# Kernel optimization log

Hardware: AMD Instinct MI355X
Metric: run time of the kernel (lower is better)

The kernel has to match this reference:

```python
import jax, jax.numpy as jnp
import numpy as np

VOCAB = 100000
HIDDEN = 512
NUM_CLUSTERS = 256
B, S = 8, 2048


def setup_inputs() -> dict:
    key = jax.random.key(0)
    k1, k2, k3, k4, k5 = jax.random.split(key, 5)
    return {
        "location_ids": jax.random.randint(k1, (B, S), 0, VOCAB),
        "fine_embed_w": jax.random.normal(k2, (VOCAB, HIDDEN // 2), dtype=jnp.float32),
        "coarse_embed_w": jax.random.normal(k3, (NUM_CLUSTERS, HIDDEN // 2), dtype=jnp.float32),
        "loc_to_cluster_w": jax.random.normal(k4, (NUM_CLUSTERS, VOCAB), dtype=jnp.float32),
        "loc_to_cluster_b": jax.random.normal(k5, (NUM_CLUSTERS,), dtype=jnp.float32),
    }


def reference(location_ids, fine_embed_w, coarse_embed_w, loc_to_cluster_w, loc_to_cluster_b):
    # fine embedding gather: [B,S,H/2]
    fine_emb = fine_embed_w[location_ids]
    # one_hot(ids) @ W^T + b  ==  gather columns of W at ids, plus bias
    # cluster_logits: [B,S,C]
    cluster_logits = loc_to_cluster_w.T[location_ids] + loc_to_cluster_b
    cluster_dist = jax.nn.softmax(cluster_logits, axis=-1)
    # soft mixture of coarse cluster embeddings: [B,S,H/2]
    coarse_emb = jnp.einsum("bsc,ch->bsh", cluster_dist, coarse_embed_w)
    return jnp.concatenate([fine_emb, coarse_emb], axis=-1)
```

## Files before the change

### kernel.cpp

```cpp
#include <hip/hip_runtime.h>
#include <hip/hip_bf16.h>

#define VOCAB 100000
#define HALF  256
#define NC    256
#define NTOK  16384
#define SEGSZ 3200
#define NSEG  32
#define NHB   16

using frag  = __attribute__((ext_vector_type(8))) short;
using f32x4 = __attribute__((ext_vector_type(4))) float;

static __device__ inline unsigned bfpk(float lo, float hi) {
    union { __hip_bfloat162 h2; unsigned u; } cv;
    cv.h2.x = __float2bfloat16(lo);
    cv.h2.y = __float2bfloat16(hi);
    return cv.u;
}

static __device__ inline void gload_lds16(const float* g, float* l) {
    __builtin_amdgcn_global_load_lds(
        (const __attribute__((address_space(1))) void*)g,
        (__attribute__((address_space(3))) void*)l, 16, 0, 0);
}

__global__ __launch_bounds__(1024)
void prep1(const int* __restrict__ ids, const float* __restrict__ coarse_w,
           int* __restrict__ partial, ushort* __restrict__ cT)
{
    __shared__ float tile[64][65];
    __shared__ int lh[NSEG];
    const int tid = threadIdx.x;
    const int b   = blockIdx.x;

    if (b < NHB) {
        if (tid < NSEG) lh[tid] = 0;
        __syncthreads();
        atomicAdd(&lh[ids[b * 1024 + tid] / SEGSZ], 1);
        __syncthreads();
        if (tid < NSEG) partial[b * NSEG + tid] = lh[tid];
    } else {
        const int bt = b - NHB;
        const int ci = (bt >> 2) * 64, hi = (bt & 3) * 64;
#pragma unroll
        for (int p = 0; p < 4; ++p) {
            const int idx = tid + p * 1024;
            const int cl = idx >> 6, hl = idx & 63;
            tile[cl][hl] = coarse_w[(size_t)(ci + cl) * HALF + hi + hl];
        }
        __syncthreads();
#pragma unroll
        for (int p = 0; p < 4; ++p) {
            const int idx = tid + p * 1024;
            const int hl = idx >> 6, cl = idx & 63;
            __hip_bfloat16 v = __float2bfloat16(tile[cl][hl]);
            cT[(size_t)(hi + hl) * NC + ci + cl] = *reinterpret_cast<ushort*>(&v);
        }
    }
}

__global__ __launch_bounds__(1024)
void prep2(const int* __restrict__ ids, const int* __restrict__ partial,
           int* __restrict__ seg_off, int* __restrict__ stok, int* __restrict__ sidv)
{
    __shared__ int part_l[NHB][NSEG];
    __shared__ int segoff[NSEG + 1];
    __shared__ int basebs[NSEG];
    __shared__ int cnt[NSEG];
    const int tid = threadIdx.x;
    const int b   = blockIdx.x;

    if (tid < NHB * NSEG) part_l[tid >> 5][tid & 31] = partial[tid];
    __syncthreads();

    if (tid < NSEG) {
        int tot_before = 0, tot_s = 0, base = 0;
        for (int bb = 0; bb < NHB; ++bb) {
            const int v = part_l[bb][tid];
            tot_s += v;
            if (bb < b) base += v;
        }
        for (int s = 0; s < NSEG; ++s)
            if (s < tid)
                for (int bb = 0; bb < NHB; ++bb) tot_before += part_l[bb][s];
        segoff[tid] = tot_before;
        basebs[tid] = base;
        cnt[tid]    = 0;
        if (tid == NSEG - 1) segoff[NSEG] = tot_before + tot_s;
    }
    __syncthreads();

    const int t  = b * 1024 + tid;
    const int id = ids[t];
    const int sg = id / SEGSZ;
    const int r  = atomicAdd(&cnt[sg], 1);
    const int pos = segoff[sg] + basebs[sg] + r;
    stok[pos] = t;
    sidv[pos] = id;

    if (b == 0 && tid <= NSEG) seg_off[tid] = segoff[tid];
}

__global__ __launch_bounds__(256)
void gather_rows(const float* __restrict__ cluster_w,
                 const float* __restrict__ cluster_b,
                 const int*   __restrict__ sidv,
                 const int*   __restrict__ seg_off,
                 __hip_bfloat16* __restrict__ logT)
{
    __shared__ float seg[3328];
    const int bid  = blockIdx.x;
    const int r    = bid >> 5;
    const int s    = bid & 31;
    const int tid  = threadIdx.x;
    const int wave = tid >> 6;
    const int lane = tid & 63;
    const int sbase = s * SEGSZ;

    const float* rowseg = cluster_w + (size_t)r * VOCAB + sbase;

    if (r == NC - 1 && s == NSEG - 1) {
        const int nf4 = (VOCAB - sbase) >> 2;
        for (int i = tid; i < nf4; i += 256)
            *reinterpret_cast<float4*>(&seg[4 * i]) =
                reinterpret_cast<const float4*>(rowseg)[i];
    } else {
        gload_lds16(rowseg + (wave)      * 256 + lane * 4, &seg[(wave)      * 256]);
        gload_lds16(rowseg + (wave + 4)  * 256 + lane * 4, &seg[(wave + 4)  * 256]);
        gload_lds16(rowseg + (wave + 8)  * 256 + lane * 4, &seg[(wave + 8)  * 256]);
        if (wave == 0)
            gload_lds16(rowseg + 12 * 256 + lane * 4, &seg[12 * 256]);
    }

    const float bias = cluster_b[r];
    const int lo = seg_off[s];
    const int hi = seg_off[s + 1];
    __syncthreads();

    for (int i = lo + tid; i < hi; i += 256)
        logT[(size_t)r * NTOK + i] = __float2bfloat16(seg[sidv[i] - sbase] + bias);
}

__global__ __launch_bounds__(512)
void mix_mfma(const ushort* __restrict__ logT,
              const float*  __restrict__ fine_w,
              const ushort* __restrict__ cT,
              const int*    __restrict__ stok,
              const int*    __restrict__ sidv,
              float*        __restrict__ out)
{
    __shared__ uint4 ldsA[32][33];
    __shared__ float redu[32][17];
    __shared__ int stok_l[32], sid_l[32];

    const int tid  = threadIdx.x;
    const int base = blockIdx.x * 32;

    if (tid < 32) { stok_l[tid] = stok[base + tid]; sid_l[tid] = sidv[base + tid]; }

    const int s = tid & 31;
    const int g = tid >> 5;
    float v[16];
#pragma unroll
    for (int i = 0; i < 16; ++i) {
        const unsigned u = logT[(size_t)(g * 16 + i) * NTOK + base + s];
        v[i] = __uint_as_float(u << 16);
    }
    float m = v[0];
#pragma unroll
    for (int i = 1; i < 16; ++i) m = fmaxf(m, v[i]);
    redu[s][g] = m;
    __syncthreads();
    float M = redu[s][0];
#pragma unroll
    for (int i = 1; i < 16; ++i) M = fmaxf(M, redu[s][i]);
    __syncthreads();
    float sum = 0.f;
#pragma unroll
    for (int i = 0; i < 16; ++i) { v[i] = __expf(v[i] - M); sum += v[i]; }
    redu[s][g] = sum;
    __syncthreads();
    float tot = 0.f;
#pragma unroll
    for (int i = 0; i < 16; ++i) tot += redu[s][i];
    const float inv = 1.f / tot;

    {
        uint4 u0, u1;
        u0.x = bfpk(v[0] * inv,  v[1] * inv);
        u0.y = bfpk(v[2] * inv,  v[3] * inv);
        u0.z = bfpk(v[4] * inv,  v[5] * inv);
        u0.w = bfpk(v[6] * inv,  v[7] * inv);
        u1.x = bfpk(v[8] * inv,  v[9] * inv);
        u1.y = bfpk(v[10] * inv, v[11] * inv);
        u1.z = bfpk(v[12] * inv, v[13] * inv);
        u1.w = bfpk(v[14] * inv, v[15] * inv);
        ldsA[s][2 * g]     = u0;
        ldsA[s][2 * g + 1] = u1;
    }

    {
        const int sl = tid >> 4, l16 = tid & 15;
        const float4* fs = reinterpret_cast<const float4*>(fine_w + (size_t)sid_l[sl] * HALF);
        float4* fd = reinterpret_cast<float4*>(out + (size_t)stok_l[sl] * 512);
#pragma unroll
        for (int p = 0; p < 4; ++p) fd[l16 + 16 * p] = fs[l16 + 16 * p];
    }
    __syncthreads();

    const int w    = tid >> 6;
    const int lane = tid & 63;
    const int arow = (w & 1) * 16 + (lane & 15);
    const int ngrp = (w >> 1) * 4;
    f32x4 acc[4];
#pragma unroll
    for (int q = 0; q < 4; ++q) acc[q] = (f32x4){0.f, 0.f, 0.f, 0.f};

    for (int ch = 0; ch < 8; ++ch) {
        const frag a = *reinterpret_cast<const frag*>(&ldsA[arow][ch * 4 + (lane >> 4)]);
#pragma unroll
        for (int q = 0; q < 4; ++q) {
            const int n = (ngrp + q) * 16 + (lane & 15);
            const frag b = *reinterpret_cast<const frag*>(
                cT + (size_t)n * NC + ch * 32 + (lane >> 4) * 8);
            acc[q] = __builtin_amdgcn_mfma_f32_16x16x32_bf16(a, b, acc[q], 0, 0, 0);
        }
    }

#pragma unroll
    for (int q = 0; q < 4; ++q) {
        const int col = (ngrp + q) * 16 + (lane & 15);
#pragma unroll
        for (int r = 0; r < 4; ++r) {
            const int srow = (w & 1) * 16 + (lane >> 4) * 4 + r;
            out[(size_t)stok_l[srow] * 512 + 256 + col] = acc[q][r];
        }
    }
}

extern "C" void kernel_launch(void* const* d_in, const int* in_sizes, int n_in,
                              void* d_out, int out_size, void* d_ws, size_t ws_size,
                              hipStream_t stream) {
    const int*   ids       = (const int*)  d_in[0];
    const float* fine_w    = (const float*)d_in[1];
    const float* coarse_w  = (const float*)d_in[2];
    const float* cluster_w = (const float*)d_in[3];
    const float* cluster_b = (const float*)d_in[4];
    float*       out       = (float*)d_out;

    int* partial = (int*)d_ws;
    int* seg_off = partial + NHB * NSEG;
    int* stok    = seg_off + 64;
    int* sidv    = stok + NTOK;
    __hip_bfloat16* logT = (__hip_bfloat16*)(sidv + NTOK);
    ushort* cT = (ushort*)(logT + (size_t)NC * NTOK);

    const size_t need = (size_t)(NHB * NSEG + 64 + 2 * NTOK) * sizeof(int)
                      + (size_t)NC * NTOK * 2 + (size_t)HALF * NC * 2;
    if (ws_size < need) return;

    hipLaunchKernelGGL(prep1, dim3(2 * NHB), dim3(1024), 0, stream,
                       ids, coarse_w, partial, cT);
    hipLaunchKernelGGL(prep2, dim3(NHB), dim3(1024), 0, stream,
                       ids, partial, seg_off, stok, sidv);
    hipLaunchKernelGGL(gather_rows, dim3(NC * NSEG), dim3(256), 0, stream,
                       cluster_w, cluster_b, sidv, seg_off, logT);
    hipLaunchKernelGGL(mix_mfma, dim3(NTOK / 32), dim3(512), 0, stream,
                       (const ushort*)logT, fine_w, cT, stok, sidv, out);
}
```

Baseline: 57.22 us.

## Double-buffer row segments in gather_rows, four segments per block

```diff
diff --git a/kernel.cpp b/kernel.cpp
--- a/kernel.cpp
+++ b/kernel.cpp
@@ -109,37 +109,61 @@
                  const int*   __restrict__ seg_off,
                  __hip_bfloat16* __restrict__ logT)
 {
-    __shared__ float seg[3328];
+    __shared__ float seg[2][3328];
     const int bid  = blockIdx.x;
-    const int r    = bid >> 5;
-    const int s    = bid & 31;
+    const int r    = bid >> 3;
+    const int e    = bid & 7;
     const int tid  = threadIdx.x;
     const int wave = tid >> 6;
     const int lane = tid & 63;
-    const int sbase = s * SEGSZ;
-
-    const float* rowseg = cluster_w + (size_t)r * VOCAB + sbase;
-
-    if (r == NC - 1 && s == NSEG - 1) {
-        const int nf4 = (VOCAB - sbase) >> 2;
-        for (int i = tid; i < nf4; i += 256)
-            *reinterpret_cast<float4*>(&seg[4 * i]) =
-                reinterpret_cast<const float4*>(rowseg)[i];
-    } else {
-        gload_lds16(rowseg + (wave)      * 256 + lane * 4, &seg[(wave)      * 256]);
-        gload_lds16(rowseg + (wave + 4)  * 256 + lane * 4, &seg[(wave + 4)  * 256]);
-        gload_lds16(rowseg + (wave + 8)  * 256 + lane * 4, &seg[(wave + 8)  * 256]);
-        if (wave == 0)
-            gload_lds16(rowseg + 12 * 256 + lane * 4, &seg[12 * 256]);
-    }
-
+    const int s0   = e * 4;
+    const bool last = (bid == 2047);
+
+    const float* rowp = cluster_w + (size_t)r * VOCAB;
     const float bias = cluster_b[r];
-    const int lo = seg_off[s];
-    const int hi = seg_off[s + 1];
-    __syncthreads();
-
-    for (int i = lo + tid; i < hi; i += 256)
-        logT[(size_t)r * NTOK + i] = __float2bfloat16(seg[sidv[i] - sbase] + bias);
+
+    int off_[5];
+#pragma unroll
+    for (int k = 0; k <= 4; ++k) off_[k] = seg_off[s0 + k];
+
+    auto issue = [&](int k, int buf, bool tail) {
+        const float* p = rowp + (size_t)(s0 + k) * SEGSZ;
+        float* l = seg[buf];
+        if (!tail) {
+            gload_lds16(p + (wave)     * 256 + lane * 4, l + (wave)     * 256);
+            gload_lds16(p + (wave + 4) * 256 + lane * 4, l + (wave + 4) * 256);
+            gload_lds16(p + (wave + 8) * 256 + lane * 4, l + (wave + 8) * 256);
+            if (wave == 0)
+                gload_lds16(p + 12 * 256 + lane * 4, l + 12 * 256);
+        } else {
+            if (wave < 3)
+                gload_lds16(p + wave * 256 + lane * 4, l + wave * 256);
+            if (tid < 32) l[768 + tid] = p[768 + tid];
+        }
+    };
+
+    issue(0, 0, false);
+
+    for (int k = 0; k < 4; ++k) {
+        if (k < 3) issue(k + 1, (k + 1) & 1, last && (k + 1) == 3);
+
+        if (last || k == 3) {
+            asm volatile("s_waitcnt vmcnt(0) lgkmcnt(0)" ::: "memory");
+        } else if (wave == 0) {
+            asm volatile("s_waitcnt vmcnt(4)" ::: "memory");
+        } else {
+            asm volatile("s_waitcnt vmcnt(3)" ::: "memory");
+        }
+        __builtin_amdgcn_sched_barrier(0);
+        __builtin_amdgcn_s_barrier();
+
+        const int sbase = (s0 + k) * SEGSZ;
+        const float* l = seg[k & 1];
+        for (int i = off_[k] + tid; i < off_[k + 1]; i += 256)
+            logT[(size_t)r * NTOK + i] = __float2bfloat16(l[sidv[i] - sbase] + bias);
+
+        __builtin_amdgcn_s_barrier();
+    }
 }
 
 __global__ __launch_bounds__(512)
@@ -264,7 +288,7 @@
                        ids, coarse_w, partial, cT);
     hipLaunchKernelGGL(prep2, dim3(NHB), dim3(1024), 0, stream,
                        ids, partial, seg_off, stok, sidv);
-    hipLaunchKernelGGL(gather_rows, dim3(NC * NSEG), dim3(256), 0, stream,
+    hipLaunchKernelGGL(gather_rows, dim3(NC * 8), dim3(256), 0, stream,
                        cluster_w, cluster_b, sidv, seg_off, logT);
     hipLaunchKernelGGL(mix_mfma, dim3(NTOK / 32), dim3(512), 0, stream,
                        (const ushort*)logT, fine_w, cT, stok, sidv, out);
```

Result: no change. 57.35 us (+0.2%).

## Pipeline per-wave double-buffered segment staging in gather_rows with power-of-two segments

Applied to the files above, without the earlier changes.

```diff
diff --git a/kernel.cpp b/kernel.cpp
--- a/kernel.cpp
+++ b/kernel.cpp
@@ -5,8 +5,9 @@
 #define HALF  256
 #define NC    256
 #define NTOK  16384
-#define SEGSZ 3200
-#define NSEG  32
+#define SEG2  1024
+#define NSEG2 100
+#define RUNS  25
 #define NHB   16
 
 using frag  = __attribute__((ext_vector_type(8))) short;
@@ -30,16 +31,16 @@
            int* __restrict__ partial, ushort* __restrict__ cT)
 {
     __shared__ float tile[64][65];
-    __shared__ int lh[NSEG];
+    __shared__ int lh[NSEG2];
     const int tid = threadIdx.x;
     const int b   = blockIdx.x;
 
     if (b < NHB) {
-        if (tid < NSEG) lh[tid] = 0;
+        if (tid < NSEG2) lh[tid] = 0;
         __syncthreads();
-        atomicAdd(&lh[ids[b * 1024 + tid] / SEGSZ], 1);
+        atomicAdd(&lh[ids[b * 1024 + tid] >> 10], 1);
         __syncthreads();
-        if (tid < NSEG) partial[b * NSEG + tid] = lh[tid];
+        if (tid < NSEG2) partial[b * NSEG2 + tid] = lh[tid];
     } else {
         const int bt = b - NHB;
         const int ci = (bt >> 2) * 64, hi = (bt & 3) * 64;
@@ -64,42 +65,47 @@
 void prep2(const int* __restrict__ ids, const int* __restrict__ partial,
            int* __restrict__ seg_off, int* __restrict__ stok, int* __restrict__ sidv)
 {
-    __shared__ int part_l[NHB][NSEG];
-    __shared__ int segoff[NSEG + 1];
-    __shared__ int basebs[NSEG];
-    __shared__ int cnt[NSEG];
+    __shared__ int part_l[NHB][NSEG2];
+    __shared__ int colt[NSEG2];
+    __shared__ int segoff[NSEG2 + 1];
+    __shared__ int basebs[NSEG2];
+    __shared__ int cnt[NSEG2];
     const int tid = threadIdx.x;
     const int b   = blockIdx.x;
 
-    if (tid < NHB * NSEG) part_l[tid >> 5][tid & 31] = partial[tid];
-    __syncthreads();
-
-    if (tid < NSEG) {
-        int tot_before = 0, tot_s = 0, base = 0;
+    for (int e = tid; e < NHB * NSEG2; e += 1024)
+        part_l[e / NSEG2][e % NSEG2] = partial[e];
+    __syncthreads();
+
+    if (tid < NSEG2) {
+        int tot_s = 0, base = 0;
         for (int bb = 0; bb < NHB; ++bb) {
             const int v = part_l[bb][tid];
             tot_s += v;
             if (bb < b) base += v;
         }
-        for (int s = 0; s < NSEG; ++s)
-            if (s < tid)
-                for (int bb = 0; bb < NHB; ++bb) tot_before += part_l[bb][s];
-        segoff[tid] = tot_before;
+        colt[tid]   = tot_s;
         basebs[tid] = base;
         cnt[tid]    = 0;
-        if (tid == NSEG - 1) segoff[NSEG] = tot_before + tot_s;
+    }
+    __syncthreads();
+    if (tid < NSEG2) {
+        int tb = 0;
+        for (int s = 0; s < tid; ++s) tb += colt[s];
+        segoff[tid] = tb;
+        if (tid == NSEG2 - 1) segoff[NSEG2] = tb + colt[tid];
     }
     __syncthreads();
 
     const int t  = b * 1024 + tid;
     const int id = ids[t];
-    const int sg = id / SEGSZ;
+    const int sg = id >> 10;
     const int r  = atomicAdd(&cnt[sg], 1);
     const int pos = segoff[sg] + basebs[sg] + r;
     stok[pos] = t;
     sidv[pos] = id;
 
-    if (b == 0 && tid <= NSEG) seg_off[tid] = segoff[tid];
+    if (b == 0 && tid <= NSEG2) seg_off[tid] = segoff[tid];
 }
 
 __global__ __launch_bounds__(256)
@@ -109,37 +115,58 @@
                  const int*   __restrict__ seg_off,
                  __hip_bfloat16* __restrict__ logT)
 {
-    __shared__ float seg[3328];
-    const int bid  = blockIdx.x;
-    const int r    = bid >> 5;
-    const int s    = bid & 31;
+    __shared__ float seg[4][2][SEG2];
     const int tid  = threadIdx.x;
-    const int wave = tid >> 6;
+    const int wv   = tid >> 6;
     const int lane = tid & 63;
-    const int sbase = s * SEGSZ;
-
-    const float* rowseg = cluster_w + (size_t)r * VOCAB + sbase;
-
-    if (r == NC - 1 && s == NSEG - 1) {
-        const int nf4 = (VOCAB - sbase) >> 2;
-        for (int i = tid; i < nf4; i += 256)
-            *reinterpret_cast<float4*>(&seg[4 * i]) =
-                reinterpret_cast<const float4*>(rowseg)[i];
-    } else {
-        gload_lds16(rowseg + (wave)      * 256 + lane * 4, &seg[(wave)      * 256]);
-        gload_lds16(rowseg + (wave + 4)  * 256 + lane * 4, &seg[(wave + 4)  * 256]);
-        gload_lds16(rowseg + (wave + 8)  * 256 + lane * 4, &seg[(wave + 8)  * 256]);
-        if (wave == 0)
-            gload_lds16(rowseg + 12 * 256 + lane * 4, &seg[12 * 256]);
-    }
-
+    const int W    = blockIdx.x * 4 + wv;
+    const int r    = W / RUNS;
+    const int run  = W - r * RUNS;
+    const int s0   = run * 4;
+
+    const float* rowp = cluster_w + (size_t)r * VOCAB;
     const float bias = cluster_b[r];
-    const int lo = seg_off[s];
-    const int hi = seg_off[s + 1];
-    __syncthreads();
-
-    for (int i = lo + tid; i < hi; i += 256)
-        logT[(size_t)r * NTOK + i] = __float2bfloat16(seg[sidv[i] - sbase] + bias);
+
+    auto nch = [&](int s) {
+        int v = VOCAB - s * SEG2;
+        v = v < 0 ? 0 : (v > SEG2 ? SEG2 : v);
+        return v >> 8;
+    };
+    auto issue = [&](int s, int buf) {
+        const int c = nch(s);
+        const float* p = rowp + s * SEG2;
+        float* l = &seg[wv][buf][0];
+        for (int k = 0; k < c; ++k)
+            gload_lds16(p + k * 256 + lane * 4, l + k * 256);
+    };
+
+    int off_[5];
+#pragma unroll
+    for (int j = 0; j <= 4; ++j) off_[j] = seg_off[s0 + j];
+
+    issue(s0, 0);
+    for (int j = 0; j < 4; ++j) {
+        const int s = s0 + j;
+        int nw = 0;
+        if (j < 3) { issue(s + 1, (j + 1) & 1); nw = nch(s + 1); }
+
+        if (nw == 4)      asm volatile("s_waitcnt vmcnt(4)" ::: "memory");
+        else if (nw == 2) asm volatile("s_waitcnt vmcnt(2)" ::: "memory");
+        else              asm volatile("s_waitcnt vmcnt(0)" ::: "memory");
+        __builtin_amdgcn_sched_barrier(0);
+
+        const int sbase  = s * SEG2;
+        const int staged = nch(s) << 8;
+        const float* l = &seg[wv][j & 1][0];
+        for (int i = off_[j] + lane; i < off_[j + 1]; i += 64) {
+            const int id  = sidv[i];
+            const int idx = id - sbase;
+            float val;
+            if (idx < staged) val = l[idx];
+            else              val = rowp[id];
+            logT[(size_t)r * NTOK + i] = __float2bfloat16(val + bias);
+        }
+    }
 }
 
 __global__ __launch_bounds__(512)
@@ -250,13 +277,13 @@
     float*       out       = (float*)d_out;
 
     int* partial = (int*)d_ws;
-    int* seg_off = partial + NHB * NSEG;
-    int* stok    = seg_off + 64;
+    int* seg_off = partial + NHB * NSEG2;
+    int* stok    = seg_off + 128;
     int* sidv    = stok + NTOK;
     __hip_bfloat16* logT = (__hip_bfloat16*)(sidv + NTOK);
     ushort* cT = (ushort*)(logT + (size_t)NC * NTOK);
 
-    const size_t need = (size_t)(NHB * NSEG + 64 + 2 * NTOK) * sizeof(int)
+    const size_t need = (size_t)(NHB * NSEG2 + 128 + 2 * NTOK) * sizeof(int)
                       + (size_t)NC * NTOK * 2 + (size_t)HALF * NC * 2;
     if (ws_size < need) return;
 
@@ -264,7 +291,7 @@
                        ids, coarse_w, partial, cT);
     hipLaunchKernelGGL(prep2, dim3(NHB), dim3(1024), 0, stream,
                        ids, partial, seg_off, stok, sidv);
-    hipLaunchKernelGGL(gather_rows, dim3(NC * NSEG), dim3(256), 0, stream,
+    hipLaunchKernelGGL(gather_rows, dim3(NC * RUNS / 4), dim3(256), 0, stream,
                        cluster_w, cluster_b, sidv, seg_off, logT);
     hipLaunchKernelGGL(mix_mfma, dim3(NTOK / 32), dim3(512), 0, stream,
                        (const ushort*)logT, fine_w, cT, stok, sidv, out);
```

Result: no change. 57.04 us (-0.3%).
